# Optimization experiments

Hardware: AMD Instinct MI355X
Metric: run time of the kernel (lower is better)

Reference implementation:

```python
import jax, jax.numpy as jnp
import numpy as np
from jax import lax

MAX_ITERS = 200
X_INNER_ITERS = 20
RHO = 1.0
X_STEP = 1e-3


def setup_inputs() -> dict:
    key = jax.random.key(0)
    k1, k2, k3 = jax.random.split(key, 3)
    m, n = 512, 1024
    # Scale A so x_step * rho * ||A^T A||_2 < 2 -> inner GD loop is stable.
    A = jax.random.normal(k1, (m, n), dtype=jnp.float32) / jnp.sqrt(jnp.float32(n))
    b = jax.random.normal(k2, (m,), dtype=jnp.float32)
    c = jax.random.normal(k3, (n,), dtype=jnp.float32)
    return {"A": A, "b": b, "c": c}


def _admm(A, b, c):
    m, n = A.shape
    x0 = jnp.zeros((n,), dtype=A.dtype)
    s0 = jnp.zeros((m,), dtype=A.dtype)
    u0 = jnp.zeros((m,), dtype=A.dtype)

    def outer_step(carry, _):
        x, s, u = carry
        r = s + b - u  # [m]

        def inner_step(xk, _):
            grad = c + RHO * (A.T @ (A @ xk - r))  # [n]
            xk = jnp.maximum(xk - X_STEP * grad, 0.0)
            return xk, None

        x, _ = lax.scan(inner_step, x, None, length=X_INNER_ITERS)
        Ax = A @ x  # [m]
        s = jnp.maximum(Ax - b + u, 0.0)
        u = u + (Ax - s - b)
        return (x, s, u), None

    (x, s, u), _ = lax.scan(outer_step, (x0, s0, u0), None, length=MAX_ITERS)
    p = RHO * u
    lambda_k = jnp.maximum(-p, 0.0)          # [m]
    nu_k = jnp.maximum(c + A.T @ p, 0.0)     # [n]
    return x, s, u, lambda_k, nu_k


def reference(A, b, c):
    # return_history=False, so x_hist is None in the original; omitted here.
    return _admm(A, b, c)
```

## Files before the change

kernel.cpp:

```cpp
#include <hip/hip_runtime.h>
#include <hip/hip_bf16.h>

#define MDIM 512
#define NDIM 1024
#define MAX_OUTER 200
#define X_INNER 20
#define RHO 1.0f
#define XSTEP 1e-3f

#define GBLK 32
#define TPB 256
#define NPER (NDIM / GBLK)
#define MPER (MDIM / GBLK)


__device__ __forceinline__ float agent_load(const float* p) {
  return __hip_atomic_load(p, __ATOMIC_RELAXED, __HIP_MEMORY_SCOPE_AGENT);
}
__device__ __forceinline__ void agent_store(float* p, float v) {
  __hip_atomic_store(p, v, __ATOMIC_RELAXED, __HIP_MEMORY_SCOPE_AGENT);
}

__device__ __forceinline__ float wave_reduce_sum(float v) {
#pragma unroll
  for (int off = 32; off > 0; off >>= 1) v += __shfl_xor(v, off, 64);
  return v;
}

__device__ __forceinline__ void grid_barrier(int* flags, int epoch, int bid) {
  __syncthreads();
  if (threadIdx.x == 0)
    __hip_atomic_store(&flags[bid * 32], epoch, __ATOMIC_RELEASE,
                       __HIP_MEMORY_SCOPE_AGENT);
  if (threadIdx.x < GBLK) {
    while (__hip_atomic_load(&flags[threadIdx.x * 32], __ATOMIC_ACQUIRE,
                             __HIP_MEMORY_SCOPE_AGENT) < epoch)
      __builtin_amdgcn_s_sleep(2);
  }
  __syncthreads();
}


#define ATA_BK 32
#define ATA_BT 64

__global__ void __launch_bounds__(256) ata_kernel(const float* __restrict__ A,
                                                  float* __restrict__ Mout) {
  __shared__ float As[ATA_BK][ATA_BT];
  __shared__ float Bs[ATA_BK][ATA_BT];
  const int bi = blockIdx.y * ATA_BT;
  const int bj = blockIdx.x * ATA_BT;
  const int tid = threadIdx.x;
  const int tx = tid & 15, ty = tid >> 4;
  float acc[4][4] = {};
  for (int k0 = 0; k0 < MDIM; k0 += ATA_BK) {
#pragma unroll
    for (int t = tid; t < ATA_BK * ATA_BT; t += 256) {
      int kk = t >> 6, ii = t & 63;
      As[kk][ii] = A[(size_t)(k0 + kk) * NDIM + bi + ii];
      Bs[kk][ii] = A[(size_t)(k0 + kk) * NDIM + bj + ii];
    }
    __syncthreads();
#pragma unroll
    for (int kk = 0; kk < ATA_BK; ++kk) {
      float a[4], bb[4];
#pragma unroll
      for (int r = 0; r < 4; ++r) a[r] = As[kk][ty * 4 + r];
#pragma unroll
      for (int r = 0; r < 4; ++r) bb[r] = Bs[kk][tx * 4 + r];
#pragma unroll
      for (int r = 0; r < 4; ++r)
#pragma unroll
        for (int q = 0; q < 4; ++q) acc[r][q] = fmaf(a[r], bb[q], acc[r][q]);
    }
    __syncthreads();
  }
#pragma unroll
  for (int r = 0; r < 4; ++r)
#pragma unroll
    for (int q = 0; q < 4; ++q)
      Mout[(size_t)(bi + ty * 4 + r) * NDIM + bj + tx * 4 + q] = acc[r][q];
}


__global__ void __launch_bounds__(TPB) admm_kernel(
    const float* __restrict__ A, const float* __restrict__ bvec,
    const float* __restrict__ cvec, const float* __restrict__ Mm,
    float* __restrict__ xg0, float* __restrict__ xg1, float* __restrict__ sg,
    float* __restrict__ ug, int* flags, float* __restrict__ out) {
  __shared__ float xs[NDIM];
  __shared__ float rs[MDIM];
  __shared__ float wl[NPER];
  __shared__ float cl[NPER];
  __shared__ float wred[NPER][9];

  const int tid = threadIdx.x;
  const int bid = blockIdx.x;
  const int wave = tid >> 6;
  const int lane = tid & 63;
  const int i0 = bid * NPER;
  const int k0 = bid * MPER;

  float* xbuf[2] = {xg0, xg1};
  int p = 0;

  if (tid < NPER) cl[tid] = cvec[i0 + tid];
  for (int j = tid; j < NDIM; j += TPB) xs[j] = 0.0f;
  __syncthreads();

  int epoch = 0;

  for (int outer = 0; outer < MAX_OUTER; ++outer) {
    for (int k = tid; k < MDIM; k += TPB)
      rs[k] = agent_load(&sg[k]) + bvec[k] - agent_load(&ug[k]);
    __syncthreads();
    {
      const int ii = tid & (NPER - 1);
      const int kg = tid >> 5;
      float pp = 0.0f;
#pragma unroll
      for (int kk = 0; kk < MDIM / 8; ++kk) {
        const int k = kg * (MDIM / 8) + kk;
        pp = fmaf(A[(size_t)k * NDIM + i0 + ii], rs[k], pp);
      }
      wred[ii][kg] = pp;
    }
    __syncthreads();
    if (tid < NPER) {
      float sum = 0.0f;
#pragma unroll
      for (int q = 0; q < 8; ++q) sum += wred[tid][q];
      wl[tid] = sum;
    }
    __syncthreads();

    for (int it = 0; it < X_INNER; ++it) {
      float* xnew = xbuf[p ^ 1];
#pragma unroll
      for (int rr = 0; rr < 8; ++rr) {
        const int ii = wave * 8 + rr;
        const int i = i0 + ii;
        const float* Mrow = Mm + (size_t)i * NDIM;
        float pp = 0.0f;
#pragma unroll
        for (int t = 0; t < NDIM / 64; ++t) {
          const int j = lane + t * 64;
          pp = fmaf(Mrow[j], xs[j], pp);
        }
        pp = wave_reduce_sum(pp);
        if (lane == 0) {
          const float g = cl[ii] + RHO * (pp - wl[ii]);
          agent_store(&xnew[i], fmaxf(xs[i] - XSTEP * g, 0.0f));
        }
      }
      ++epoch;
      grid_barrier(flags, epoch, bid);
      for (int j = tid; j < NDIM; j += TPB) xs[j] = agent_load(&xnew[j]);
      p ^= 1;
      __syncthreads();
    }

#pragma unroll
    for (int rr = 0; rr < 4; ++rr) {
      const int k = k0 + wave * 4 + rr;
      const float* Arow = A + (size_t)k * NDIM;
      float pp = 0.0f;
#pragma unroll
      for (int t = 0; t < NDIM / 64; ++t) {
        const int j = lane + t * 64;
        pp = fmaf(Arow[j], xs[j], pp);
      }
      pp = wave_reduce_sum(pp);
      if (lane == 0) {
        const float uk = agent_load(&ug[k]);
        const float bk = bvec[k];
        const float sv = fmaxf(pp - bk + uk, 0.0f);
        agent_store(&sg[k], sv);
        agent_store(&ug[k], uk + pp - sv - bk);
      }
    }
    ++epoch;
    grid_barrier(flags, epoch, bid);
  }

  if (tid < NPER) out[i0 + tid] = xs[i0 + tid];
  if (tid < MPER) {
    const int k = k0 + tid;
    const float sv = agent_load(&sg[k]);
    const float uv = agent_load(&ug[k]);
    out[NDIM + k] = sv;
    out[NDIM + MDIM + k] = uv;
    out[NDIM + 2 * MDIM + k] = fmaxf(-RHO * uv, 0.0f);
  }
  for (int k = tid; k < MDIM; k += TPB) rs[k] = agent_load(&ug[k]);
  __syncthreads();
  {
    const int ii = tid & (NPER - 1);
    const int kg = tid >> 5;
    float pp = 0.0f;
#pragma unroll
    for (int kk = 0; kk < MDIM / 8; ++kk) {
      const int k = kg * (MDIM / 8) + kk;
      pp = fmaf(A[(size_t)k * NDIM + i0 + ii], rs[k], pp);
    }
    wred[ii][kg] = pp;
  }
  __syncthreads();
  if (tid < NPER) {
    float t = 0.0f;
#pragma unroll
    for (int q = 0; q < 8; ++q) t += wred[tid][q];
    out[NDIM + 3 * MDIM + i0 + tid] = fmaxf(cl[tid] + RHO * t, 0.0f);
  }
}


extern "C" void kernel_launch(void* const* d_in, const int* in_sizes, int n_in,
                              void* d_out, int out_size, void* d_ws,
                              size_t ws_size, hipStream_t stream) {
  const float* A = (const float*)d_in[0];
  const float* b = (const float*)d_in[1];
  const float* c = (const float*)d_in[2];
  float* out = (float*)d_out;

  float* Mws = (float*)d_ws;
  float* xg0 = Mws + (size_t)NDIM * NDIM;
  float* xg1 = xg0 + NDIM;
  float* sg = xg1 + NDIM;
  float* ug = sg + MDIM;
  int* flags = (int*)(ug + MDIM);

  hipMemsetAsync(xg0, 0,
                 (2 * NDIM + 2 * MDIM) * sizeof(float) +
                     GBLK * 32 * sizeof(int),
                 stream);

  dim3 g1(NDIM / ATA_BT, NDIM / ATA_BT);
  ata_kernel<<<g1, 256, 0, stream>>>(A, Mws);
  admm_kernel<<<GBLK, TPB, 0, stream>>>(A, b, c, Mws, xg0, xg1, sg, ug, flags,
                                        out);
}
```

Baseline: 21.12 ms.

## Cache M row slice in LDS, hold x in registers, spin barrier without sleep

Each block now loads its 32 rows of A^T A into shared memory once (128KB as float4) rather than streaming them from global memory on every inner iteration. The x vector is kept in per-lane registers with float4-strided access, and each block's own x entries are tracked in registers, so the shared xs array and one syncthreads per iteration go away. The grid barrier now spins with relaxed loads and no sleep, followed by a single acquire fence. The large LDS allocation limits occupancy to one block per CU, and busy spinning adds memory traffic while blocks wait.

```diff
diff --git a/kernel.cpp b/kernel.cpp
--- a/kernel.cpp
+++ b/kernel.cpp
@@ -1,5 +1,4 @@
 #include <hip/hip_runtime.h>
-#include <hip/hip_bf16.h>
 
 #define MDIM 512
 #define NDIM 1024
@@ -33,11 +32,12 @@
     __hip_atomic_store(&flags[bid * 32], epoch, __ATOMIC_RELEASE,
                        __HIP_MEMORY_SCOPE_AGENT);
   if (threadIdx.x < GBLK) {
-    while (__hip_atomic_load(&flags[threadIdx.x * 32], __ATOMIC_ACQUIRE,
-                             __HIP_MEMORY_SCOPE_AGENT) < epoch)
-      __builtin_amdgcn_s_sleep(2);
-  }
-  __syncthreads();
+    while (__hip_atomic_load(&flags[threadIdx.x * 32], __ATOMIC_RELAXED,
+                             __HIP_MEMORY_SCOPE_AGENT) < epoch) {
+    }
+  }
+  __syncthreads();
+  __builtin_amdgcn_fence(__ATOMIC_ACQUIRE, "agent");
 }
 
 
@@ -88,7 +88,7 @@
     const float* __restrict__ cvec, const float* __restrict__ Mm,
     float* __restrict__ xg0, float* __restrict__ xg1, float* __restrict__ sg,
     float* __restrict__ ug, int* flags, float* __restrict__ out) {
-  __shared__ float xs[NDIM];
+  __shared__ float4 Ml4[NPER][NDIM / 4];
   __shared__ float rs[MDIM];
   __shared__ float wl[NPER];
   __shared__ float cl[NPER];
@@ -101,14 +101,26 @@
   const int i0 = bid * NPER;
   const int k0 = bid * MPER;
 
-  float* xbuf[2] = {xg0, xg1};
-  int p = 0;
-
+  {
+    const float4* Msrc = (const float4*)(Mm + (size_t)i0 * NDIM);
+    float4* Mdst = &Ml4[0][0];
+    for (int f = tid; f < NPER * NDIM / 4; f += TPB) Mdst[f] = Msrc[f];
+  }
   if (tid < NPER) cl[tid] = cvec[i0 + tid];
-  for (int j = tid; j < NDIM; j += TPB) xs[j] = 0.0f;
-  __syncthreads();
-
+
+  float xr[4][4];
+#pragma unroll
+  for (int t = 0; t < 4; ++t)
+#pragma unroll
+    for (int q = 0; q < 4; ++q) xr[t][q] = 0.0f;
+  float ox[8];
+#pragma unroll
+  for (int r = 0; r < 8; ++r) ox[r] = 0.0f;
+
+  float* xa = xg0;
+  float* xb = xg1;
   int epoch = 0;
+  __syncthreads();
 
   for (int outer = 0; outer < MAX_OUTER; ++outer) {
     for (int k = tid; k < MDIM; k += TPB)
@@ -135,40 +147,57 @@
     __syncthreads();
 
     for (int it = 0; it < X_INNER; ++it) {
-      float* xnew = xbuf[p ^ 1];
-#pragma unroll
-      for (int rr = 0; rr < 8; ++rr) {
-        const int ii = wave * 8 + rr;
-        const int i = i0 + ii;
-        const float* Mrow = Mm + (size_t)i * NDIM;
-        float pp = 0.0f;
-#pragma unroll
-        for (int t = 0; t < NDIM / 64; ++t) {
-          const int j = lane + t * 64;
-          pp = fmaf(Mrow[j], xs[j], pp);
+      float acc[8];
+#pragma unroll
+      for (int r = 0; r < 8; ++r) acc[r] = 0.0f;
+#pragma unroll
+      for (int r = 0; r < 8; ++r) {
+        const int rl = wave * 8 + r;
+#pragma unroll
+        for (int t = 0; t < 4; ++t) {
+          const float4 m = Ml4[rl][lane + 64 * t];
+          acc[r] = fmaf(m.x, xr[t][0], acc[r]);
+          acc[r] = fmaf(m.y, xr[t][1], acc[r]);
+          acc[r] = fmaf(m.z, xr[t][2], acc[r]);
+          acc[r] = fmaf(m.w, xr[t][3], acc[r]);
         }
-        pp = wave_reduce_sum(pp);
-        if (lane == 0) {
-          const float g = cl[ii] + RHO * (pp - wl[ii]);
-          agent_store(&xnew[i], fmaxf(xs[i] - XSTEP * g, 0.0f));
+      }
+#pragma unroll
+      for (int r = 0; r < 8; ++r) acc[r] = wave_reduce_sum(acc[r]);
+      if (lane == 0) {
+#pragma unroll
+        for (int r = 0; r < 8; ++r) {
+          const int ii = wave * 8 + r;
+          const float g = cl[ii] + RHO * (acc[r] - wl[ii]);
+          const float xn = fmaxf(ox[r] - XSTEP * g, 0.0f);
+          ox[r] = xn;
+          agent_store(&xb[i0 + ii], xn);
         }
       }
       ++epoch;
       grid_barrier(flags, epoch, bid);
-      for (int j = tid; j < NDIM; j += TPB) xs[j] = agent_load(&xnew[j]);
-      p ^= 1;
-      __syncthreads();
-    }
-
-#pragma unroll
-    for (int rr = 0; rr < 4; ++rr) {
-      const int k = k0 + wave * 4 + rr;
-      const float* Arow = A + (size_t)k * NDIM;
+#pragma unroll
+      for (int t = 0; t < 4; ++t)
+#pragma unroll
+        for (int q = 0; q < 4; ++q)
+          xr[t][q] = agent_load(&xb[4 * lane + 256 * t + q]);
+      float* tmp = xa;
+      xa = xb;
+      xb = tmp;
+    }
+
+#pragma unroll
+    for (int r = 0; r < 4; ++r) {
+      const int k = k0 + wave * 4 + r;
+      const float4* Arow4 = (const float4*)(A + (size_t)k * NDIM);
       float pp = 0.0f;
 #pragma unroll
-      for (int t = 0; t < NDIM / 64; ++t) {
-        const int j = lane + t * 64;
-        pp = fmaf(Arow[j], xs[j], pp);
+      for (int t = 0; t < 4; ++t) {
+        const float4 a = Arow4[lane + 64 * t];
+        pp = fmaf(a.x, xr[t][0], pp);
+        pp = fmaf(a.y, xr[t][1], pp);
+        pp = fmaf(a.z, xr[t][2], pp);
+        pp = fmaf(a.w, xr[t][3], pp);
       }
       pp = wave_reduce_sum(pp);
       if (lane == 0) {
@@ -183,7 +212,7 @@
     grid_barrier(flags, epoch, bid);
   }
 
-  if (tid < NPER) out[i0 + tid] = xs[i0 + tid];
+  if (tid < NPER) out[i0 + tid] = agent_load(&xa[i0 + tid]);
   if (tid < MPER) {
     const int k = k0 + tid;
     const float sv = agent_load(&sg[k]);
```

Result: slower. 23.09 ms (+9.3%).
